# Kernel tuning notes

Hardware: AMD Instinct MI355X
Metric: run time of the kernel (lower is better)

## Reference

```python
import jax, jax.numpy as jnp
import numpy as np

H, B, M, D = 2, 2048, 64, 16
N_ENT, N_REL = 500000, 32


def setup_inputs() -> dict:
    key = jax.random.key(0)
    k1, k2, k3, k4, k5, k6 = jax.random.split(key, 6)
    items = jax.random.randint(k1, (B,), 0, N_ENT)
    heads = jax.random.randint(k2, (H, B, M), 0, N_ENT)
    relations = jax.random.randint(k3, (H, B, M), 0, N_REL)
    tails = jax.random.randint(k4, (H, B, M), 0, N_ENT)
    ent_emb = jax.random.normal(k5, (N_ENT, D), dtype=jnp.float32) * 0.1
    rel_emb = jax.random.normal(k6, (N_REL, D, D), dtype=jnp.float32) * 0.1
    return {"items": items, "heads": heads, "relations": relations,
            "tails": tails, "ent_emb": ent_emb, "rel_emb": rel_emb}


def reference(items, heads, relations, tails, ent_emb, rel_emb):
    # gathers over ragged-as-dense ripple sets
    item_e = ent_emb[items]        # [B, D]
    head_e = ent_emb[heads]        # [H, B, M, D]
    rel_e = rel_emb[relations]     # [H, B, M, D, D]
    tail_e = ent_emb[tails]        # [H, B, M, D]
    # Rh = R @ h  -> [H, B, M, D]
    Rh = jnp.einsum('hbmij,hbmj->hbmi', rel_e, head_e)
    # attention logits hRv = Rh . v (item embedding) -> [H, B, M]
    hRv = jnp.einsum('hbmi,bi->hbm', Rh, item_e)
    pi = jax.nn.softmax(hRv, axis=2)          # softmax over memory dim (dim=1 in torch per hop)
    # weighted tail aggregation, summed over hops -> [B, D]
    user_rep = jnp.einsum('hbm,hbmd->bd', pi, tail_e)
    predicts = jax.nn.sigmoid(jnp.sum(user_rep * item_e, axis=1))  # [B]
    return predicts
```

## Files before the change

kernel.cpp:

```cpp
#include <hip/hip_runtime.h>
#include <math.h>

#define HOPS 2
#define BATCH 2048
#define MEM 64
#define DIM 16
#define NREL 32

__global__ __launch_bounds__(512)
void ripple_kernel(const int* __restrict__ items,
                   const int* __restrict__ heads,
                   const int* __restrict__ relations,
                   const int* __restrict__ tails,
                   const float* __restrict__ ent_emb,
                   const float* __restrict__ rel_emb,
                   float* __restrict__ out)
{
    const int b    = blockIdx.x;
    const int tid  = threadIdx.x;
    const int g    = tid >> 2;
    const int sub  = tid & 3;
    const int h    = g >> 6;
    const int m    = g & 63;
    const int wave = tid >> 6;

    __shared__ float s_item[DIM];
    __shared__ float s_itemR[NREL * DIM];
    __shared__ float s_max[8];
    __shared__ float s_num[8];
    __shared__ float s_den[8];

    const int base = h * (BATCH * MEM) + b * MEM + m;
    const int hidx = heads[base];
    const int ridx = relations[base];
    const int tidx = tails[base];

    if (tid < 4) {
        float4 v = ((const float4*)(ent_emb + (size_t)items[b] * DIM))[tid];
        ((float4*)s_item)[tid] = v;
    }
    __syncthreads();

    const float4 hseg = *(const float4*)(ent_emb + (size_t)hidx * DIM + sub * 4);
    const float4 tseg = *(const float4*)(ent_emb + (size_t)tidx * DIM + sub * 4);

    {
        const int r = tid >> 4;
        const int j = tid & 15;
        const float* Rp = rel_emb + r * (DIM * DIM) + j;
        float acc = 0.0f;
        #pragma unroll
        for (int i = 0; i < DIM; ++i)
            acc = fmaf(s_item[i], Rp[i * DIM], acc);
        s_itemR[(r << 4) + j] = acc;
    }
    __syncthreads();

    const float4 irseg = *((const float4*)(s_itemR + (ridx << 4)) + sub);
    const float4 iseg  = ((const float4*)s_item)[sub];

    float lpart = hseg.x * irseg.x + hseg.y * irseg.y +
                  hseg.z * irseg.z + hseg.w * irseg.w;
    float tpart = tseg.x * iseg.x + tseg.y * iseg.y +
                  tseg.z * iseg.z + tseg.w * iseg.w;

    lpart += __shfl_xor(lpart, 1, 64);
    lpart += __shfl_xor(lpart, 2, 64);

    float mx = lpart;
    #pragma unroll
    for (int off = 4; off < 64; off <<= 1)
        mx = fmaxf(mx, __shfl_xor(mx, off, 64));
    if ((tid & 63) == 0) s_max[wave] = mx;
    __syncthreads();
    const int hb = (wave >> 2) << 2;
    mx = fmaxf(fmaxf(s_max[hb], s_max[hb + 1]),
               fmaxf(s_max[hb + 2], s_max[hb + 3]));

    const float e   = __expf(lpart - mx);
    float num = e * tpart;
    float den = e * 0.25f;
    #pragma unroll
    for (int off = 1; off < 64; off <<= 1) {
        num += __shfl_xor(num, off, 64);
        den += __shfl_xor(den, off, 64);
    }
    if ((tid & 63) == 0) { s_num[wave] = num; s_den[wave] = den; }
    __syncthreads();

    if (tid == 0) {
        const float n0 = s_num[0] + s_num[1] + s_num[2] + s_num[3];
        const float d0 = s_den[0] + s_den[1] + s_den[2] + s_den[3];
        const float n1 = s_num[4] + s_num[5] + s_num[6] + s_num[7];
        const float d1 = s_den[4] + s_den[5] + s_den[6] + s_den[7];
        const float x = n0 / d0 + n1 / d1;
        out[b] = 1.0f / (1.0f + __expf(-x));
    }
}

extern "C" void kernel_launch(void* const* d_in, const int* in_sizes, int n_in,
                              void* d_out, int out_size, void* d_ws, size_t ws_size,
                              hipStream_t stream) {
    const int*   items     = (const int*)d_in[0];
    const int*   heads     = (const int*)d_in[1];
    const int*   relations = (const int*)d_in[2];
    const int*   tails     = (const int*)d_in[3];
    const float* ent_emb   = (const float*)d_in[4];
    const float* rel_emb   = (const float*)d_in[5];
    float*       out       = (float*)d_out;

    ripple_kernel<<<BATCH, 512, 0, stream>>>(items, heads, relations, tails,
                                             ent_emb, rel_emb, out);
}
```

Baseline: 89.06 us.

## Process four batch rows per block, one thread per memory slot, drop softmax max

Each block now handles four batch rows, with one thread per (hop, memory) slot loading full 16-float head and tail rows. This replaces four threads per slot working on float4 segments. The item-times-relation table is computed for all four items in one pass, so each relation matrix load is shared across them. The softmax max-subtraction pass and its barrier are removed, which relies on the logits being small enough that exp does not overflow. That is an input-range assumption which could break on other data.

```diff
diff --git a/kernel.cpp b/kernel.cpp
--- a/kernel.cpp
+++ b/kernel.cpp
@@ -6,6 +6,7 @@
 #define MEM 64
 #define DIM 16
 #define NREL 32
+#define BPB 4
 
 __global__ __launch_bounds__(512)
 void ripple_kernel(const int* __restrict__ items,
@@ -16,85 +17,86 @@
                    const float* __restrict__ rel_emb,
                    float* __restrict__ out)
 {
-    const int b    = blockIdx.x;
     const int tid  = threadIdx.x;
-    const int g    = tid >> 2;
-    const int sub  = tid & 3;
-    const int h    = g >> 6;
-    const int m    = g & 63;
+    const int b0   = blockIdx.x * BPB;
+    const int bl   = tid >> 7;
+    const int h    = (tid >> 6) & 1;
+    const int m    = tid & 63;
     const int wave = tid >> 6;
+    const int b    = b0 + bl;
 
-    __shared__ float s_item[DIM];
-    __shared__ float s_itemR[NREL * DIM];
-    __shared__ float s_max[8];
-    __shared__ float s_num[8];
-    __shared__ float s_den[8];
+    __shared__ float s_item[BPB][DIM];
+    __shared__ float s_itemR[BPB][NREL][DIM];
+    __shared__ float s_num[2 * BPB];
+    __shared__ float s_den[2 * BPB];
 
     const int base = h * (BATCH * MEM) + b * MEM + m;
     const int hidx = heads[base];
     const int ridx = relations[base];
     const int tidx = tails[base];
 
-    if (tid < 4) {
-        float4 v = ((const float4*)(ent_emb + (size_t)items[b] * DIM))[tid];
-        ((float4*)s_item)[tid] = v;
+    const float4* hp = (const float4*)(ent_emb + (size_t)hidx * DIM);
+    const float4* tp = (const float4*)(ent_emb + (size_t)tidx * DIM);
+    const float4 h0 = hp[0], h1 = hp[1], h2 = hp[2], h3 = hp[3];
+    const float4 t0 = tp[0], t1 = tp[1], t2 = tp[2], t3 = tp[3];
+
+    if (tid < 4 * BPB) {
+        const int ib  = tid >> 2;
+        const int seg = tid & 3;
+        ((float4*)s_item[ib])[seg] =
+            ((const float4*)(ent_emb + (size_t)items[b0 + ib] * DIM))[seg];
     }
     __syncthreads();
-
-    const float4 hseg = *(const float4*)(ent_emb + (size_t)hidx * DIM + sub * 4);
-    const float4 tseg = *(const float4*)(ent_emb + (size_t)tidx * DIM + sub * 4);
 
     {
         const int r = tid >> 4;
         const int j = tid & 15;
         const float* Rp = rel_emb + r * (DIM * DIM) + j;
-        float acc = 0.0f;
+        float acc0 = 0.f, acc1 = 0.f, acc2 = 0.f, acc3 = 0.f;
         #pragma unroll
-        for (int i = 0; i < DIM; ++i)
-            acc = fmaf(s_item[i], Rp[i * DIM], acc);
-        s_itemR[(r << 4) + j] = acc;
+        for (int i = 0; i < DIM; ++i) {
+            const float v = Rp[i * DIM];
+            acc0 = fmaf(s_item[0][i], v, acc0);
+            acc1 = fmaf(s_item[1][i], v, acc1);
+            acc2 = fmaf(s_item[2][i], v, acc2);
+            acc3 = fmaf(s_item[3][i], v, acc3);
+        }
+        s_itemR[0][r][j] = acc0;
+        s_itemR[1][r][j] = acc1;
+        s_itemR[2][r][j] = acc2;
+        s_itemR[3][r][j] = acc3;
     }
     __syncthreads();
 
-    const float4 irseg = *((const float4*)(s_itemR + (ridx << 4)) + sub);
-    const float4 iseg  = ((const float4*)s_item)[sub];
+    const float4* irp = (const float4*)s_itemR[bl][ridx];
+    const float4 r0 = irp[0], r1 = irp[1], r2 = irp[2], r3 = irp[3];
+    const float4* ipl = (const float4*)s_item[bl];
+    const float4 i0 = ipl[0], i1 = ipl[1], i2 = ipl[2], i3 = ipl[3];
 
-    float lpart = hseg.x * irseg.x + hseg.y * irseg.y +
-                  hseg.z * irseg.z + hseg.w * irseg.w;
-    float tpart = tseg.x * iseg.x + tseg.y * iseg.y +
-                  tseg.z * iseg.z + tseg.w * iseg.w;
+    float logit = h0.x*r0.x + h0.y*r0.y + h0.z*r0.z + h0.w*r0.w
+                + h1.x*r1.x + h1.y*r1.y + h1.z*r1.z + h1.w*r1.w
+                + h2.x*r2.x + h2.y*r2.y + h2.z*r2.z + h2.w*r2.w
+                + h3.x*r3.x + h3.y*r3.y + h3.z*r3.z + h3.w*r3.w;
+    float tdot  = t0.x*i0.x + t0.y*i0.y + t0.z*i0.z + t0.w*i0.w
+                + t1.x*i1.x + t1.y*i1.y + t1.z*i1.z + t1.w*i1.w
+                + t2.x*i2.x + t2.y*i2.y + t2.z*i2.z + t2.w*i2.w
+                + t3.x*i3.x + t3.y*i3.y + t3.z*i3.z + t3.w*i3.w;
 
-    lpart += __shfl_xor(lpart, 1, 64);
-    lpart += __shfl_xor(lpart, 2, 64);
-
-    float mx = lpart;
-    #pragma unroll
-    for (int off = 4; off < 64; off <<= 1)
-        mx = fmaxf(mx, __shfl_xor(mx, off, 64));
-    if ((tid & 63) == 0) s_max[wave] = mx;
-    __syncthreads();
-    const int hb = (wave >> 2) << 2;
-    mx = fmaxf(fmaxf(s_max[hb], s_max[hb + 1]),
-               fmaxf(s_max[hb + 2], s_max[hb + 3]));
-
-    const float e   = __expf(lpart - mx);
-    float num = e * tpart;
-    float den = e * 0.25f;
+    const float e = __expf(logit);
+    float num = e * tdot;
+    float den = e;
     #pragma unroll
     for (int off = 1; off < 64; off <<= 1) {
         num += __shfl_xor(num, off, 64);
         den += __shfl_xor(den, off, 64);
     }
-    if ((tid & 63) == 0) { s_num[wave] = num; s_den[wave] = den; }
+    if (m == 0) { s_num[wave] = num; s_den[wave] = den; }
     __syncthreads();
 
-    if (tid == 0) {
-        const float n0 = s_num[0] + s_num[1] + s_num[2] + s_num[3];
-        const float d0 = s_den[0] + s_den[1] + s_den[2] + s_den[3];
-        const float n1 = s_num[4] + s_num[5] + s_num[6] + s_num[7];
-        const float d1 = s_den[4] + s_den[5] + s_den[6] + s_den[7];
-        const float x = n0 / d0 + n1 / d1;
-        out[b] = 1.0f / (1.0f + __expf(-x));
+    if (tid < BPB) {
+        const float x = s_num[2*tid]     / s_den[2*tid]
+                      + s_num[2*tid + 1] / s_den[2*tid + 1];
+        out[b0 + tid] = 1.0f / (1.0f + __expf(-x));
     }
 }
 
@@ -109,6 +111,6 @@
     const float* rel_emb   = (const float*)d_in[5];
     float*       out       = (float*)d_out;
 
-    ripple_kernel<<<BATCH, 512, 0, stream>>>(items, heads, relations, tails,
-                                             ent_emb, rel_emb, out);
+    ripple_kernel<<<BATCH / BPB, 512, 0, stream>>>(items, heads, relations,
+                                                   tails, ent_emb, rel_emb, out);
 }
```

After: 89.60 us. About the same (+0.6%).
